# Kernel optimization log

Measured on AMD Instinct MI355X. Metric: run time of the kernel, lower is better.

Reference implementation:

```python
import jax, jax.numpy as jnp
import numpy as np

L, N, IN, H, K, OUT = 512, 256, 256, 512, 2, 256


def setup_inputs() -> dict:
    key = jax.random.key(0)
    ks = jax.random.split(key, 14)
    s = 1.0 / np.sqrt(H)
    u = lambda k, shape: jax.random.uniform(k, shape, jnp.float32, -s, s)
    return {
        'x': jax.random.normal(ks[0], (L, N, IN), jnp.float32),
        'memory': jax.random.normal(ks[1], (N, K * H), jnp.float32) * 0.1,
        'done': jax.random.bernoulli(ks[2], 0.01, (L, N, 1)),
        'Wih0': u(ks[3], (3 * H, IN)),
        'Whh0': u(ks[4], (3 * H, H)),
        'bih0': u(ks[5], (3 * H,)),
        'bhh0': u(ks[6], (3 * H,)),
        'Wih1': u(ks[7], (3 * H, H)),
        'Whh1': u(ks[8], (3 * H, H)),
        'bih1': u(ks[9], (3 * H,)),
        'bhh1': u(ks[10], (3 * H,)),
        'Wp': u(ks[11], (OUT, H)),
        'bp': u(ks[12], (OUT,)),
    }


def _gru_layer(xs, h0, done_f, Wih, Whh, bih, bhh):
    # xs: [L, N, C_in], h0: [N, H], done_f: [L, N, 1] float
    def step(h, inp):
        x_t, d_t = inp
        gi = x_t @ Wih.T + bih            # [N, 3H]
        gh = h @ Whh.T + bhh              # [N, 3H]
        i_r, i_z, i_n = jnp.split(gi, 3, axis=-1)
        h_r, h_z, h_n = jnp.split(gh, 3, axis=-1)
        r = jax.nn.sigmoid(i_r + h_r)
        z = jax.nn.sigmoid(i_z + h_z)
        n = jnp.tanh(i_n + r * h_n)
        h_new = (1.0 - z) * n + z * h     # torch GRU update
        # reset state AFTER an episode terminates at step t (affects t+1)
        h_carry = h_new * (1.0 - d_t)
        return h_carry, h_new
    hT, ys = jax.lax.scan(step, h0, (xs, done_f))
    return ys, hT


def reference(x, memory, done, Wih0, Whh0, bih0, bhh0, Wih1, Whh1, bih1, bhh1, Wp, bp):
    done_f = done.astype(x.dtype)                       # [L, N, 1]
    # memory: 'n (k c) -> k n c'
    h0 = jnp.transpose(memory.reshape(memory.shape[0], K, H), (1, 0, 2))
    y0, h0f = _gru_layer(x, h0[0], done_f, Wih0, Whh0, bih0, bhh0)
    y1, h1f = _gru_layer(y0, h0[1], done_f, Wih1, Whh1, bih1, bhh1)
    # hn: 'k n c -> n (k c)'
    hn = jnp.transpose(jnp.stack([h0f, h1f], 0), (1, 0, 2)).reshape(memory.shape[0], K * H)
    out = y1 @ Wp.T + bp                                # output projection
    return out, hn
```

## Files before the change

kernel.cpp:

```cpp
#include <hip/hip_runtime.h>

static constexpr int LSEQ = 512;
static constexpr int NB   = 256;
static constexpr int CIN  = 256;
static constexpr int HD   = 512;
static constexpr int G3   = 1536;
static constexpr int NOUT = 256;

typedef __attribute__((ext_vector_type(8))) short bf16x8;
typedef __attribute__((ext_vector_type(4))) float f32x4;
typedef __attribute__((ext_vector_type(8))) unsigned short u16x8;
typedef __attribute__((ext_vector_type(4))) unsigned u32x4;

#define DEVI __device__ __forceinline__

DEVI float b2f(unsigned short h) { return __uint_as_float(((unsigned)h) << 16); }
DEVI unsigned short f2b(float x) {
    unsigned u = __float_as_uint(x);
    return (unsigned short)((u + 0x7FFFu + ((u >> 16) & 1u)) >> 16);
}

DEVI unsigned cload(const unsigned* p) {
    return __hip_atomic_load(p, __ATOMIC_RELAXED, __HIP_MEMORY_SCOPE_AGENT);
}
DEVI void cstore(unsigned* p, unsigned v) {
    __hip_atomic_store(p, v, __ATOMIC_RELAXED, __HIP_MEMORY_SCOPE_AGENT);
}

DEVI float fast_tanh(float x) {
    x = fminf(10.f, fmaxf(-10.f, x));
    float e = __expf(-2.f * x);
    return (1.f - e) / (1.f + e);
}

DEVI void cload4x4(const unsigned* p0, const unsigned* p1,
                   const unsigned* p2, const unsigned* p3,
                   u32x4& r0, u32x4& r1, u32x4& r2, u32x4& r3) {
    asm volatile(
        "global_load_dwordx4 %0, %4, off sc0 sc1\n\t"
        "global_load_dwordx4 %1, %5, off sc0 sc1\n\t"
        "global_load_dwordx4 %2, %6, off sc0 sc1\n\t"
        "global_load_dwordx4 %3, %7, off sc0 sc1\n\t"
        "s_waitcnt vmcnt(0)"
        : "=&v"(r0), "=&v"(r1), "=&v"(r2), "=&v"(r3)
        : "v"(p0), "v"(p1), "v"(p2), "v"(p3)
        : "memory");
    __builtin_amdgcn_sched_barrier(0);
}

__global__ void detect_fdt(const unsigned short* __restrict__ x, int nHalf,
                           unsigned* __restrict__ fdt) {
    __shared__ unsigned big;
    if (threadIdx.x == 0) big = 0;
    __syncthreads();
    for (int i = threadIdx.x; i < nHalf; i += 256) {
        unsigned e = (x[i] >> 7) & 0xFFu;
        if (e >= 0xC0u) atomicOr(&big, 1u);
    }
    __syncthreads();
    if (threadIdx.x == 0) *fdt = big ? 1u : 0u;
}

__global__ void cast_bf16(const void* __restrict__ src, long srcOff,
                          unsigned short* __restrict__ dst, long n,
                          const unsigned* __restrict__ fdt) {
    long i = (long)blockIdx.x * 256 + threadIdx.x;
    long stride = (long)gridDim.x * 256;
    if (*fdt) {
        const float* s = (const float*)src + srcOff;
        for (; i < n; i += stride) dst[i] = f2b(s[i]);
    } else {
        const unsigned short* s = (const unsigned short*)src + srcOff;
        for (; i < n; i += stride) dst[i] = s[i];
    }
}

__global__ void detect_done(const unsigned char* __restrict__ d, int elems,
                            unsigned* __restrict__ flag) {
    __shared__ unsigned bad[4];
    int tid = threadIdx.x;
    if (tid < 4) bad[tid] = 0;
    __syncthreads();
    int nInt = elems >> 2;
    const unsigned* di = (const unsigned*)d;
    for (int i = tid; i < nInt; i += 256) {
        unsigned v = di[i];
        if (v > 1u) atomicOr(&bad[0], 1u);
        if (v != 0u && v != 0x3F800000u) atomicOr(&bad[1], 1u);
    }
    int nHalf = elems >> 1;
    const unsigned short* dh = (const unsigned short*)d;
    for (int i = tid; i < nHalf; i += 256) {
        unsigned short h = dh[i];
        if (h != 0 && h != 0x3F80) atomicOr(&bad[2], 1u);
    }
    __syncthreads();
    if (tid == 0) {
        unsigned f;
        if (!bad[0]) f = 0u;
        else if (!bad[1]) f = 3u;
        else if (!bad[2]) f = 2u;
        else f = 1u;
        *flag = f;
    }
}

__global__ void expand_done(const void* __restrict__ d, const unsigned* __restrict__ flag,
                            float* __restrict__ keep, int elems) {
    int i = blockIdx.x * 256 + threadIdx.x;
    if (i >= elems) return;
    unsigned f = *flag;
    float v;
    if (f == 0u)      v = (float)((const int*)d)[i];
    else if (f == 1u) v = (float)((const unsigned char*)d)[i];
    else if (f == 2u) v = b2f(((const unsigned short*)d)[i]);
    else              v = ((const float*)d)[i];
    keep[i] = 1.f - v;
}

__global__ __launch_bounds__(256) void gemm_nt(
    const unsigned short* __restrict__ A, const unsigned short* __restrict__ B,
    const unsigned short* __restrict__ bias, unsigned short* __restrict__ C,
    float* __restrict__ Cf, const unsigned* __restrict__ fdt,
    int M, int N, int K) {
    __shared__ unsigned short sm[16384];
    const int tid = threadIdx.x;
    const int l = tid & 63, w = tid >> 6;
    const int lr = l & 15, lq = l >> 4;
    const int wr = w >> 1, wc = w & 1;
    const long rowBase = (long)blockIdx.y * 128;
    const long colBase = (long)blockIdx.x * 128;

    int qrow[4], qc8[4];
#pragma unroll
    for (int i = 0; i < 4; i++) {
        int q = (i * 4 + w) * 64 + l;
        qrow[i] = q >> 3;
        qc8[i] = (q & 7) * 8;
    }

    f32x4 acc[4][4] = {};

    for (int k0 = 0; k0 < K; k0 += 64) {
#pragma unroll
        for (int i = 0; i < 4; i++) {
            const unsigned short* sA = A + (rowBase + qrow[i]) * K + k0 + qc8[i];
            const unsigned short* sB = B + (colBase + qrow[i]) * K + k0 + qc8[i];
            __builtin_amdgcn_global_load_lds(
                (const __attribute__((address_space(1))) void*)sA,
                (__attribute__((address_space(3))) void*)(sm + (i * 4 + w) * 512), 16, 0, 0);
            __builtin_amdgcn_global_load_lds(
                (const __attribute__((address_space(1))) void*)sB,
                (__attribute__((address_space(3))) void*)(sm + 8192 + (i * 4 + w) * 512), 16, 0, 0);
        }
        __syncthreads();
#pragma unroll
        for (int ks = 0; ks < 2; ks++) {
            bf16x8 af[4], bfr[4];
#pragma unroll
            for (int mi = 0; mi < 4; mi++)
                af[mi] = *(const bf16x8*)&sm[(wr * 64 + mi * 16 + lr) * 64 + ks * 32 + lq * 8];
#pragma unroll
            for (int ni = 0; ni < 4; ni++)
                bfr[ni] = *(const bf16x8*)&sm[8192 + (wc * 64 + ni * 16 + lr) * 64 + ks * 32 + lq * 8];
#pragma unroll
            for (int mi = 0; mi < 4; mi++)
#pragma unroll
                for (int ni = 0; ni < 4; ni++)
                    acc[mi][ni] = __builtin_amdgcn_mfma_f32_16x16x32_bf16(
                        af[mi], bfr[ni], acc[mi][ni], 0, 0, 0);
        }
        __syncthreads();
    }

    float bv[4];
#pragma unroll
    for (int ni = 0; ni < 4; ni++)
        bv[ni] = bias ? b2f(bias[colBase + wc * 64 + ni * 16 + lr]) : 0.f;

    const bool f32out = (fdt != nullptr) && (*fdt != 0u);
    if (f32out) {
#pragma unroll
        for (int mi = 0; mi < 4; mi++)
#pragma unroll
            for (int ni = 0; ni < 4; ni++)
#pragma unroll
                for (int rg = 0; rg < 4; rg++) {
                    int m = wr * 64 + mi * 16 + lq * 4 + rg;
                    int n = wc * 64 + ni * 16 + lr;
                    Cf[(rowBase + m) * (long)N + colBase + n] = acc[mi][ni][rg] + bv[ni];
                }
        return;
    }

#pragma unroll
    for (int mi = 0; mi < 4; mi++)
#pragma unroll
        for (int ni = 0; ni < 4; ni++)
#pragma unroll
            for (int rg = 0; rg < 4; rg++) {
                int m = wr * 64 + mi * 16 + lq * 4 + rg;
                int n = wc * 64 + ni * 16 + lr;
                sm[m * 128 + n] = f2b(acc[mi][ni][rg] + bv[ni]);
            }
    __syncthreads();
#pragma unroll
    for (int i = 0; i < 8; i++) {
        int idx = i * 2048 + tid * 8;
        int r = idx >> 7, c = idx & 127;
        *(u16x8*)(C + (rowBase + r) * N + colBase + c) = *(const u16x8*)&sm[idx];
    }
}

DEVI void gru_body(
    const unsigned short* __restrict__ gi,
    const unsigned short* __restrict__ Whh,
    const unsigned short* __restrict__ bhh,
    const float* __restrict__ keep,
    const unsigned short* __restrict__ mem,
    unsigned short* __restrict__ hdb,
    unsigned short* __restrict__ Y,
    unsigned short* __restrict__ hnB, float* __restrict__ hnF,
    bool f32out, int t0, int Tc, int layerOff,
    unsigned* __restrict__ ctr, int lb) {
    const int tid = threadIdx.x;
    const int l = tid & 63, w = tid >> 6, lr = l & 15, lq = l >> 4;
    const int bi = lb & 15, bj = lb >> 4;

    __shared__ float red[4][16][100];

    bf16x8 wreg[6][4];
#pragma unroll
    for (int fr = 0; fr < 6; fr++) {
        int g = fr >> 1, cf = fr & 1;
        long row = (long)g * HD + bj * 32 + cf * 16 + lr;
#pragma unroll
        for (int ks = 0; ks < 4; ks++) {
            int k = w * 128 + ks * 32 + lq * 8;
            wreg[fr][ks] = *(const bf16x8*)(Whh + row * HD + k);
        }
    }

    const int m = tid >> 4, c0 = (tid & 15) * 2;
    const int n_g = bi * 16 + m;
    const int ch = bj * 32 + c0;
    float bh[3][2];
#pragma unroll
    for (int g = 0; g < 3; g++) {
        unsigned v = *(const unsigned*)(bhh + g * HD + ch);
        bh[g][0] = b2f((unsigned short)(v & 0xffffu));
        bh[g][1] = b2f((unsigned short)(v >> 16));
    }

    if (t0 == 0) {
        unsigned v = *(const unsigned*)(mem + (long)n_g * 1024 + layerOff + ch);
        cstore((unsigned*)(hdb + (long)n_g * HD + ch), v);
        unsigned* islot = ctr + ((long)Tc * 16 + bi) * 32;
        __syncthreads();
        if (tid == 0) {
            __hip_atomic_fetch_add(islot, 1u, __ATOMIC_RELAXED, __HIP_MEMORY_SCOPE_AGENT);
            while (__hip_atomic_load(islot, __ATOMIC_RELAXED, __HIP_MEMORY_SCOPE_AGENT) < 16u)
                __builtin_amdgcn_s_sleep(1);
        }
        __syncthreads();
    }

    float hpv[2];
    {
        unsigned hp0 = cload((const unsigned*)(hdb + (long)(t0 & 1) * NB * HD + (long)n_g * HD + ch));
        hpv[0] = b2f((unsigned short)(hp0 & 0xffffu));
        hpv[1] = b2f((unsigned short)(hp0 >> 16));
    }

    unsigned gv[3];
    float kp;
    {
        const unsigned short* gp = gi + (long)n_g * G3;
#pragma unroll
        for (int g = 0; g < 3; g++) gv[g] = *(const unsigned*)(gp + g * HD + ch);
        kp = keep[(long)t0 * NB + n_g];
    }

    for (int t = t0; t < t0 + Tc; ++t) {
        const unsigned short* hc = hdb + (long)(t & 1) * NB * HD;
        unsigned short* hx = hdb + (long)((t + 1) & 1) * NB * HD;

        const unsigned* hrow = (const unsigned*)(hc + (long)(bi * 16 + lr) * HD);
        union { u32x4 u; bf16x8 v; } t0u, t1u, t2u, t3u;
        cload4x4(hrow + w * 64 + 0 * 16 + lq * 4, hrow + w * 64 + 1 * 16 + lq * 4,
                 hrow + w * 64 + 2 * 16 + lq * 4, hrow + w * 64 + 3 * 16 + lq * 4,
                 t0u.u, t1u.u, t2u.u, t3u.u);
        bf16x8 af[4] = { t0u.v, t1u.v, t2u.v, t3u.v };

        f32x4 acc[6] = {};
#pragma unroll
        for (int ks = 0; ks < 4; ks++)
#pragma unroll
            for (int fr = 0; fr < 6; fr++)
                acc[fr] = __builtin_amdgcn_mfma_f32_16x16x32_bf16(af[ks], wreg[fr][ks], acc[fr], 0, 0, 0);

#pragma unroll
        for (int fr = 0; fr < 6; fr++)
#pragma unroll
            for (int rg = 0; rg < 4; rg++)
                red[w][lq * 4 + rg][fr * 16 + lr] = acc[fr][rg];
        __syncthreads();

        float s[3][2];
#pragma unroll
        for (int g = 0; g < 3; g++) { s[g][0] = 0.f; s[g][1] = 0.f; }
#pragma unroll
        for (int ww = 0; ww < 4; ww++)
#pragma unroll
            for (int g = 0; g < 3; g++) {
                const float* p = &red[ww][m][g * 32 + c0];
                s[g][0] += p[0];
                s[g][1] += p[1];
            }

        unsigned short yo[2], ho[2];
        float hcf[2];
#pragma unroll
        for (int j = 0; j < 2; j++) {
            float ir  = b2f((unsigned short)((gv[0] >> (16 * j)) & 0xffffu));
            float iz  = b2f((unsigned short)((gv[1] >> (16 * j)) & 0xffffu));
            float in_ = b2f((unsigned short)((gv[2] >> (16 * j)) & 0xffffu));
            float r = 1.f / (1.f + __expf(-(ir + s[0][j] + bh[0][j])));
            float z = 1.f / (1.f + __expf(-(iz + s[1][j] + bh[1][j])));
            float nn = fast_tanh(in_ + r * (s[2][j] + bh[2][j]));
            float hnew = (1.f - z) * nn + z * hpv[j];
            hcf[j] = hnew * kp;
            yo[j] = f2b(hnew);
            ho[j] = f2b(hcf[j]);
            hpv[j] = b2f(ho[j]);
        }
        unsigned ypack = (unsigned)yo[0] | ((unsigned)yo[1] << 16);
        unsigned hpack = (unsigned)ho[0] | ((unsigned)ho[1] << 16);

        cstore((unsigned*)(hx + (long)n_g * HD + ch), hpack);

        const bool last = (t + 1 >= t0 + Tc);
        unsigned* slot = ctr + ((long)(t - t0) * 16 + bi) * 32;
        if (!last) {
            __syncthreads();
            if (tid == 0)
                __hip_atomic_fetch_add(slot, 1u, __ATOMIC_RELAXED, __HIP_MEMORY_SCOPE_AGENT);
        }

        *(unsigned*)(Y + ((long)(t - t0) * NB + n_g) * HD + ch) = ypack;
        if (t == LSEQ - 1) {
            if (f32out) {
                hnF[(long)n_g * 1024 + layerOff + ch]     = hcf[0];
                hnF[(long)n_g * 1024 + layerOff + ch + 1] = hcf[1];
            } else {
                *(unsigned*)(hnB + (long)n_g * 1024 + layerOff + ch) = hpack;
            }
        }
        if (!last) {
            const unsigned short* gp = gi + ((long)(t + 1 - t0) * NB + n_g) * G3;
#pragma unroll
            for (int g = 0; g < 3; g++) gv[g] = *(const unsigned*)(gp + g * HD + ch);
            kp = keep[(long)(t + 1) * NB + n_g];
            if (tid == 0) {
                while (__hip_atomic_load(slot, __ATOMIC_RELAXED, __HIP_MEMORY_SCOPE_AGENT) < 16u)
                    __builtin_amdgcn_s_sleep(1);
            }
            __syncthreads();
        }
    }
}

__global__ __launch_bounds__(256, 2) void gru_dual(
    const unsigned short* giA, const unsigned short* WhhA, const unsigned short* bhhA,
    unsigned short* hdbA, unsigned short* YA, int t0A, unsigned* ctrA, int enA,
    const unsigned short* giB, const unsigned short* WhhB, const unsigned short* bhhB,
    unsigned short* hdbB, unsigned short* YB, int t0B, unsigned* ctrB, int enB,
    const float* keep, const unsigned short* mem,
    unsigned short* hnB, float* hnF, const unsigned* fdt, int Tc) {
    const bool f32out = (*fdt != 0u);
    const int half = blockIdx.x >> 8;
    const int lb = blockIdx.x & 255;
    if (half == 0) {
        if (enA) gru_body(giA, WhhA, bhhA, keep, mem, hdbA, YA, hnB, hnF,
                          f32out, t0A, Tc, 0, ctrA, lb);
    } else {
        if (enB) gru_body(giB, WhhB, bhhB, keep, mem, hdbB, YB, hnB, hnF,
                          f32out, t0B, Tc, HD, ctrB, lb);
    }
}

extern "C" void kernel_launch(void* const* d_in, const int* in_sizes, int n_in,
                              void* d_out, int out_size, void* d_ws, size_t ws_size,
                              hipStream_t stream) {
    const void* x    = d_in[0];
    const void* mem  = d_in[1];
    const void* done = d_in[2];
    const void* fsrc[11] = { mem, d_in[3], d_in[4], d_in[5], d_in[6],
                             d_in[7], d_in[8], d_in[9], d_in[10], d_in[11], d_in[12] };
    const long  fn[11]   = { (long)NB * 1024, (long)G3 * CIN, (long)G3 * HD, G3, G3,
                             (long)G3 * HD, (long)G3 * HD, G3, G3, (long)NOUT * HD, NOUT };

    unsigned short* outB = (unsigned short*)d_out;
    float*          outF = (float*)d_out;
    unsigned short* hnB  = outB + (size_t)LSEQ * NB * NOUT;
    float*          hnF  = outF + (size_t)LSEQ * NB * NOUT;

    char* ws = (char*)d_ws;
    const size_t oFlag = 0;
    const size_t oKeep = 256;
    const size_t oCtr  = oKeep + (size_t)LSEQ * NB * 4;
    const size_t oWC   = oCtr + (size_t)8 * 1024 * 1024;
    size_t wcTot = 0;
    size_t wcOff[11];
    for (int i = 0; i < 11; i++) { wcOff[i] = wcTot; wcTot += (size_t)fn[i] * 2; wcTot = (wcTot + 255) & ~(size_t)255; }
    const size_t oHdb0 = oWC + wcTot;
    const size_t oHdb1 = oHdb0 + (size_t)2 * NB * HD * 2;
    const size_t oDyn  = oHdb1 + (size_t)2 * NB * HD * 2;

    int Tc = 4;
    const int cand[6] = {128, 64, 32, 16, 8, 4};
    for (int i = 0; i < 6; i++) {
        size_t need = oDyn + (size_t)cand[i] * NB * (CIN + 2 * G3 + 2 * HD) * 2;
        if (need <= ws_size) { Tc = cand[i]; break; }
    }
    const size_t oXC  = oDyn;
    const size_t oGI0 = oXC + (size_t)Tc * NB * CIN * 2;
    const size_t oGI1 = oGI0 + (size_t)Tc * NB * G3 * 2;
    const size_t oY0c = oGI1 + (size_t)Tc * NB * G3 * 2;
    const size_t oY1c = oY0c + (size_t)Tc * NB * HD * 2;

    unsigned*       FDT  = (unsigned*)(ws + oFlag);
    unsigned*       DFLG = (unsigned*)(ws + oFlag + 64);
    float*          KEEP = (float*)(ws + oKeep);
    unsigned*       CTR  = (unsigned*)(ws + oCtr);
    unsigned short* WC   = (unsigned short*)(ws + oWC);
    unsigned short* HDB0 = (unsigned short*)(ws + oHdb0);
    unsigned short* HDB1 = (unsigned short*)(ws + oHdb1);
    unsigned short* XC   = (unsigned short*)(ws + oXC);
    unsigned short* GI0  = (unsigned short*)(ws + oGI0);
    unsigned short* GI1  = (unsigned short*)(ws + oGI1);
    unsigned short* Y0c  = (unsigned short*)(ws + oY0c);
    unsigned short* Y1c  = (unsigned short*)(ws + oY1c);

    unsigned short* MEMc = WC + wcOff[0] / 2;
    unsigned short* WIH0 = WC + wcOff[1] / 2;
    unsigned short* WHH0 = WC + wcOff[2] / 2;
    unsigned short* BIH0 = WC + wcOff[3] / 2;
    unsigned short* BHH0 = WC + wcOff[4] / 2;
    unsigned short* WIH1 = WC + wcOff[5] / 2;
    unsigned short* WHH1 = WC + wcOff[6] / 2;
    unsigned short* BIH1 = WC + wcOff[7] / 2;
    unsigned short* BHH1 = WC + wcOff[8] / 2;
    unsigned short* WPc  = WC + wcOff[9] / 2;
    unsigned short* BPc  = WC + wcOff[10] / 2;

    hipMemsetAsync(ws + oCtr, 0, (size_t)8 * 1024 * 1024, stream);
    detect_fdt<<<1, 256, 0, stream>>>((const unsigned short*)x, 4096, FDT);
    detect_done<<<1, 256, 0, stream>>>((const unsigned char*)done, in_sizes[2], DFLG);
    expand_done<<<(LSEQ * NB + 255) / 256, 256, 0, stream>>>(done, DFLG, KEEP, LSEQ * NB);

    for (int i = 0; i < 11; i++) {
        int blocks = (int)((fn[i] + 1023) / 1024);
        if (blocks > 2048) blocks = 2048;
        cast_bf16<<<blocks, 256, 0, stream>>>(fsrc[i], 0, WC + wcOff[i] / 2, fn[i], FDT);
    }

    const int NC = LSEQ / Tc;
    const size_t SZ = (size_t)(Tc + 2) * 16 * 32;
    const long giN = (long)Tc * NB * CIN;

    cast_bf16<<<2048, 256, 0, stream>>>(x, 0, XC, giN, FDT);
    gemm_nt<<<dim3(G3 / 128, Tc * NB / 128), 256, 0, stream>>>(
        XC, WIH0, BIH0, GI0, nullptr, nullptr, Tc * NB, G3, CIN);

    for (int it = 0; it <= NC; ++it) {
        const int cA = it, cB = it - 1;
        const int enA = (cA < NC) ? 1 : 0;
        const int enB = (cB >= 0) ? 1 : 0;

        gru_dual<<<512, 256, 0, stream>>>(
            GI0, WHH0, BHH0, HDB0, Y0c, cA * Tc, CTR + (size_t)(2 * it) * SZ, enA,
            GI1, WHH1, BHH1, HDB1, Y1c, cB * Tc, CTR + (size_t)(2 * it + 1) * SZ, enB,
            KEEP, MEMc, hnB, hnF, FDT, Tc);

        if (enA)
            gemm_nt<<<dim3(G3 / 128, Tc * NB / 128), 256, 0, stream>>>(
                Y0c, WIH1, BIH1, GI1, nullptr, nullptr, Tc * NB, G3, HD);
        if (enB)
            gemm_nt<<<dim3(NOUT / 128, Tc * NB / 128), 256, 0, stream>>>(
                Y1c, WPc, BPc, outB + (size_t)cB * Tc * NB * NOUT,
                outF + (size_t)cB * Tc * NB * NOUT, FDT, Tc * NB, NOUT, HD);
        if (cA + 1 < NC) {
            cast_bf16<<<2048, 256, 0, stream>>>(x, (long)(cA + 1) * Tc * NB * CIN, XC, giN, FDT);
            gemm_nt<<<dim3(G3 / 128, Tc * NB / 128), 256, 0, stream>>>(
                XC, WIH0, BIH0, GI0, nullptr, nullptr, Tc * NB, G3, CIN);
        }
    }
}
```

Baseline: 2.448 ms.

## Fuse input-projection GEMMs into the recurrent GRU kernel with register-resident Wih

Result: slower. 2.553 ms (+4.3%).

```diff
diff --git a/kernel.cpp b/kernel.cpp
--- a/kernel.cpp
+++ b/kernel.cpp
@@ -27,6 +27,7 @@
     __hip_atomic_store(p, v, __ATOMIC_RELAXED, __HIP_MEMORY_SCOPE_AGENT);
 }
 
+DEVI float sigm(float v) { return 1.f / (1.f + __expf(-v)); }
 DEVI float fast_tanh(float x) {
     x = fminf(10.f, fmaxf(-10.f, x));
     float e = __expf(-2.f * x);
@@ -212,24 +213,24 @@
     }
 }
 
+template <int KV>
 DEVI void gru_body(
-    const unsigned short* __restrict__ gi,
-    const unsigned short* __restrict__ Whh,
-    const unsigned short* __restrict__ bhh,
-    const float* __restrict__ keep,
-    const unsigned short* __restrict__ mem,
-    unsigned short* __restrict__ hdb,
-    unsigned short* __restrict__ Y,
+    const void* __restrict__ vin,
+    int vF32, int vT0off,
+    const unsigned short* __restrict__ wih,
+    const unsigned short* __restrict__ whh,
+    const unsigned short* __restrict__ bih, const unsigned short* __restrict__ bhh,
+    const float* __restrict__ keep, const unsigned short* __restrict__ mem,
+    unsigned short* __restrict__ hdb, unsigned short* __restrict__ Y,
     unsigned short* __restrict__ hnB, float* __restrict__ hnF,
     bool f32out, int t0, int Tc, int layerOff,
-    unsigned* __restrict__ ctr, int lb) {
+    unsigned* __restrict__ ctr, int lb, float (*red)[16][132]) {
+    constexpr int KVR = KV / 128;
     const int tid = threadIdx.x;
     const int l = tid & 63, w = tid >> 6, lr = l & 15, lq = l >> 4;
     const int bi = lb & 15, bj = lb >> 4;
 
-    __shared__ float red[4][16][100];
-
-    bf16x8 wreg[6][4];
+    bf16x8 wreg[6][4], wi[6][KVR];
 #pragma unroll
     for (int fr = 0; fr < 6; fr++) {
         int g = fr >> 1, cf = fr & 1;
@@ -237,19 +238,28 @@
 #pragma unroll
         for (int ks = 0; ks < 4; ks++) {
             int k = w * 128 + ks * 32 + lq * 8;
-            wreg[fr][ks] = *(const bf16x8*)(Whh + row * HD + k);
+            wreg[fr][ks] = *(const bf16x8*)(whh + row * HD + k);
+        }
+#pragma unroll
+        for (int ks = 0; ks < KVR; ks++) {
+            int k2 = w * (KV / 4) + ks * 32 + lq * 8;
+            wi[fr][ks] = *(const bf16x8*)(wih + row * KV + k2);
         }
     }
 
     const int m = tid >> 4, c0 = (tid & 15) * 2;
     const int n_g = bi * 16 + m;
     const int ch = bj * 32 + c0;
-    float bh[3][2];
-#pragma unroll
-    for (int g = 0; g < 3; g++) {
-        unsigned v = *(const unsigned*)(bhh + g * HD + ch);
-        bh[g][0] = b2f((unsigned short)(v & 0xffffu));
-        bh[g][1] = b2f((unsigned short)(v >> 16));
+    float brz[2][2], bnx[2], bnh[2];
+#pragma unroll
+    for (int g = 0; g < 2; g++)
+#pragma unroll
+        for (int j = 0; j < 2; j++)
+            brz[g][j] = b2f(bih[g * HD + ch + j]) + b2f(bhh[g * HD + ch + j]);
+#pragma unroll
+    for (int j = 0; j < 2; j++) {
+        bnx[j] = b2f(bih[2 * HD + ch + j]);
+        bnh[j] = b2f(bhh[2 * HD + ch + j]);
     }
 
     if (t0 == 0) {
@@ -272,14 +282,32 @@
         hpv[1] = b2f((unsigned short)(hp0 >> 16));
     }
 
-    unsigned gv[3];
+    auto loadV = [&](int t, bf16x8* vf) {
+        long rowoff = ((long)(t - vT0off) * NB + bi * 16 + lr);
+        int kb = w * (KV / 4) + lq * 8;
+        if (!vF32) {
+            const unsigned short* vp = (const unsigned short*)vin + rowoff * KV + kb;
+#pragma unroll
+            for (int i = 0; i < KVR; i++) vf[i] = *(const bf16x8*)(vp + i * 32);
+        } else {
+            const float* vp = (const float*)vin + rowoff * KV + kb;
+#pragma unroll
+            for (int i = 0; i < KVR; i++) {
+                f32x4 a = *(const f32x4*)(vp + i * 32);
+                f32x4 b = *(const f32x4*)(vp + i * 32 + 4);
+#pragma unroll
+                for (int e = 0; e < 4; e++) {
+                    ((unsigned short*)&vf[i])[e]     = f2b(a[e]);
+                    ((unsigned short*)&vf[i])[4 + e] = f2b(b[e]);
+                }
+            }
+        }
+    };
+
+    bf16x8 vf[KVR];
     float kp;
-    {
-        const unsigned short* gp = gi + (long)n_g * G3;
-#pragma unroll
-        for (int g = 0; g < 3; g++) gv[g] = *(const unsigned*)(gp + g * HD + ch);
-        kp = keep[(long)t0 * NB + n_g];
-    }
+    loadV(t0, vf);
+    kp = keep[(long)t0 * NB + n_g];
 
     for (int t = t0; t < t0 + Tc; ++t) {
         const unsigned short* hc = hdb + (long)(t & 1) * NB * HD;
@@ -292,42 +320,48 @@
                  t0u.u, t1u.u, t2u.u, t3u.u);
         bf16x8 af[4] = { t0u.v, t1u.v, t2u.v, t3u.v };
 
-        f32x4 acc[6] = {};
+        f32x4 acc[8] = {};
 #pragma unroll
         for (int ks = 0; ks < 4; ks++)
 #pragma unroll
-            for (int fr = 0; fr < 6; fr++)
-                acc[fr] = __builtin_amdgcn_mfma_f32_16x16x32_bf16(af[ks], wreg[fr][ks], acc[fr], 0, 0, 0);
-
-#pragma unroll
-        for (int fr = 0; fr < 6; fr++)
+            for (int fr = 0; fr < 6; fr++) {
+                int g = fr >> 1, cf = fr & 1;
+                int dst = (g < 2) ? fr : (4 + cf);
+                acc[dst] = __builtin_amdgcn_mfma_f32_16x16x32_bf16(af[ks], wreg[fr][ks], acc[dst], 0, 0, 0);
+            }
+#pragma unroll
+        for (int ks = 0; ks < KVR; ks++)
+#pragma unroll
+            for (int fr = 0; fr < 6; fr++) {
+                int g = fr >> 1, cf = fr & 1;
+                int dst = (g < 2) ? fr : (6 + cf);
+                acc[dst] = __builtin_amdgcn_mfma_f32_16x16x32_bf16(vf[ks], wi[fr][ks], acc[dst], 0, 0, 0);
+            }
+
+#pragma unroll
+        for (int f = 0; f < 8; f++)
 #pragma unroll
             for (int rg = 0; rg < 4; rg++)
-                red[w][lq * 4 + rg][fr * 16 + lr] = acc[fr][rg];
+                red[w][lq * 4 + rg][f * 16 + lr] = acc[f][rg];
         __syncthreads();
 
-        float s[3][2];
-#pragma unroll
-        for (int g = 0; g < 3; g++) { s[g][0] = 0.f; s[g][1] = 0.f; }
-#pragma unroll
-        for (int ww = 0; ww < 4; ww++)
-#pragma unroll
-            for (int g = 0; g < 3; g++) {
-                const float* p = &red[ww][m][g * 32 + c0];
-                s[g][0] += p[0];
-                s[g][1] += p[1];
-            }
+        float sr[2] = {0, 0}, sz[2] = {0, 0}, snh[2] = {0, 0}, snx[2] = {0, 0};
+#pragma unroll
+        for (int ww = 0; ww < 4; ww++) {
+            const float* p = &red[ww][m][0];
+            sr[0] += p[c0];       sr[1] += p[c0 + 1];
+            sz[0] += p[32 + c0];  sz[1] += p[33 + c0];
+            snh[0] += p[64 + c0]; snh[1] += p[65 + c0];
+            snx[0] += p[96 + c0]; snx[1] += p[97 + c0];
+        }
 
         unsigned short yo[2], ho[2];
         float hcf[2];
 #pragma unroll
         for (int j = 0; j < 2; j++) {
-            float ir  = b2f((unsigned short)((gv[0] >> (16 * j)) & 0xffffu));
-            float iz  = b2f((unsigned short)((gv[1] >> (16 * j)) & 0xffffu));
-            float in_ = b2f((unsigned short)((gv[2] >> (16 * j)) & 0xffffu));
-            float r = 1.f / (1.f + __expf(-(ir + s[0][j] + bh[0][j])));
-            float z = 1.f / (1.f + __expf(-(iz + s[1][j] + bh[1][j])));
-            float nn = fast_tanh(in_ + r * (s[2][j] + bh[2][j]));
+            float r = sigm(sr[j] + brz[0][j]);
+            float z = sigm(sz[j] + brz[1][j]);
+            float nn = fast_tanh((snx[j] + bnx[j]) + r * (snh[j] + bnh[j]));
             float hnew = (1.f - z) * nn + z * hpv[j];
             hcf[j] = hnew * kp;
             yo[j] = f2b(hnew);
@@ -357,9 +391,7 @@
             }
         }
         if (!last) {
-            const unsigned short* gp = gi + ((long)(t + 1 - t0) * NB + n_g) * G3;
-#pragma unroll
-            for (int g = 0; g < 3; g++) gv[g] = *(const unsigned*)(gp + g * HD + ch);
+            loadV(t + 1, vf);
             kp = keep[(long)(t + 1) * NB + n_g];
             if (tid == 0) {
                 while (__hip_atomic_load(slot, __ATOMIC_RELAXED, __HIP_MEMORY_SCOPE_AGENT) < 16u)
@@ -371,21 +403,28 @@
 }
 
 __global__ __launch_bounds__(256, 2) void gru_dual(
-    const unsigned short* giA, const unsigned short* WhhA, const unsigned short* bhhA,
+    const void* xin,
+    const unsigned short* WIH0, const unsigned short* WHH0,
+    const unsigned short* BIH0, const unsigned short* BHH0,
     unsigned short* hdbA, unsigned short* YA, int t0A, unsigned* ctrA, int enA,
-    const unsigned short* giB, const unsigned short* WhhB, const unsigned short* bhhB,
+    const unsigned short* y0prev,
+    const unsigned short* WIH1, const unsigned short* WHH1,
+    const unsigned short* BIH1, const unsigned short* BHH1,
     unsigned short* hdbB, unsigned short* YB, int t0B, unsigned* ctrB, int enB,
     const float* keep, const unsigned short* mem,
     unsigned short* hnB, float* hnF, const unsigned* fdt, int Tc) {
+    __shared__ float red[4][16][132];
     const bool f32out = (*fdt != 0u);
     const int half = blockIdx.x >> 8;
     const int lb = blockIdx.x & 255;
     if (half == 0) {
-        if (enA) gru_body(giA, WhhA, bhhA, keep, mem, hdbA, YA, hnB, hnF,
-                          f32out, t0A, Tc, 0, ctrA, lb);
+        if (enA) gru_body<CIN>(xin, f32out ? 1 : 0, 0, WIH0, WHH0, BIH0, BHH0,
+                               keep, mem, hdbA, YA, hnB, hnF, f32out,
+                               t0A, Tc, 0, ctrA, lb, red);
     } else {
-        if (enB) gru_body(giB, WhhB, bhhB, keep, mem, hdbB, YB, hnB, hnF,
-                          f32out, t0B, Tc, HD, ctrB, lb);
+        if (enB) gru_body<HD>(y0prev, 0, t0B, WIH1, WHH1, BIH1, BHH1,
+                              keep, mem, hdbB, YB, hnB, hnF, f32out,
+                              t0B, Tc, HD, ctrB, lb, red);
     }
 }
 
@@ -420,14 +459,12 @@
     int Tc = 4;
     const int cand[6] = {128, 64, 32, 16, 8, 4};
     for (int i = 0; i < 6; i++) {
-        size_t need = oDyn + (size_t)cand[i] * NB * (CIN + 2 * G3 + 2 * HD) * 2;
+        size_t need = oDyn + (size_t)3 * cand[i] * NB * HD * 2;
         if (need <= ws_size) { Tc = cand[i]; break; }
     }
-    const size_t oXC  = oDyn;
-    const size_t oGI0 = oXC + (size_t)Tc * NB * CIN * 2;
-    const size_t oGI1 = oGI0 + (size_t)Tc * NB * G3 * 2;
-    const size_t oY0c = oGI1 + (size_t)Tc * NB * G3 * 2;
-    const size_t oY1c = oY0c + (size_t)Tc * NB * HD * 2;
+    const size_t oY0A = oDyn;
+    const size_t oY0B = oY0A + (size_t)Tc * NB * HD * 2;
+    const size_t oY1  = oY0B + (size_t)Tc * NB * HD * 2;
 
     unsigned*       FDT  = (unsigned*)(ws + oFlag);
     unsigned*       DFLG = (unsigned*)(ws + oFlag + 64);
@@ -436,11 +473,9 @@
     unsigned short* WC   = (unsigned short*)(ws + oWC);
     unsigned short* HDB0 = (unsigned short*)(ws + oHdb0);
     unsigned short* HDB1 = (unsigned short*)(ws + oHdb1);
-    unsigned short* XC   = (unsigned short*)(ws + oXC);
-    unsigned short* GI0  = (unsigned short*)(ws + oGI0);
-    unsigned short* GI1  = (unsigned short*)(ws + oGI1);
-    unsigned short* Y0c  = (unsigned short*)(ws + oY0c);
-    unsigned short* Y1c  = (unsigned short*)(ws + oY1c);
+    unsigned short* Y0A  = (unsigned short*)(ws + oY0A);
+    unsigned short* Y0B  = (unsigned short*)(ws + oY0B);
+    unsigned short* Y1c  = (unsigned short*)(ws + oY1);
 
     unsigned short* MEMc = WC + wcOff[0] / 2;
     unsigned short* WIH0 = WC + wcOff[1] / 2;
@@ -467,33 +502,24 @@
 
     const int NC = LSEQ / Tc;
     const size_t SZ = (size_t)(Tc + 2) * 16 * 32;
-    const long giN = (long)Tc * NB * CIN;
-
-    cast_bf16<<<2048, 256, 0, stream>>>(x, 0, XC, giN, FDT);
-    gemm_nt<<<dim3(G3 / 128, Tc * NB / 128), 256, 0, stream>>>(
-        XC, WIH0, BIH0, GI0, nullptr, nullptr, Tc * NB, G3, CIN);
 
     for (int it = 0; it <= NC; ++it) {
         const int cA = it, cB = it - 1;
         const int enA = (cA < NC) ? 1 : 0;
         const int enB = (cB >= 0) ? 1 : 0;
+        unsigned short* YA = (cA & 1) ? Y0B : Y0A;
+        const unsigned short* VB = (cB & 1) ? Y0B : Y0A;
 
         gru_dual<<<512, 256, 0, stream>>>(
-            GI0, WHH0, BHH0, HDB0, Y0c, cA * Tc, CTR + (size_t)(2 * it) * SZ, enA,
-            GI1, WHH1, BHH1, HDB1, Y1c, cB * Tc, CTR + (size_t)(2 * it + 1) * SZ, enB,
+            x, WIH0, WHH0, BIH0, BHH0, HDB0, YA, cA * Tc,
+            CTR + (size_t)(2 * it) * SZ, enA,
+            VB, WIH1, WHH1, BIH1, BHH1, HDB1, Y1c, cB * Tc,
+            CTR + (size_t)(2 * it + 1) * SZ, enB,
             KEEP, MEMc, hnB, hnF, FDT, Tc);
 
-        if (enA)
-            gemm_nt<<<dim3(G3 / 128, Tc * NB / 128), 256, 0, stream>>>(
-                Y0c, WIH1, BIH1, GI1, nullptr, nullptr, Tc * NB, G3, HD);
         if (enB)
             gemm_nt<<<dim3(NOUT / 128, Tc * NB / 128), 256, 0, stream>>>(
                 Y1c, WPc, BPc, outB + (size_t)cB * Tc * NB * NOUT,
                 outF + (size_t)cB * Tc * NB * NOUT, FDT, Tc * NB, NOUT, HD);
-        if (cA + 1 < NC) {
-            cast_bf16<<<2048, 256, 0, stream>>>(x, (long)(cA + 1) * Tc * NB * CIN, XC, giN, FDT);
-            gemm_nt<<<dim3(G3 / 128, Tc * NB / 128), 256, 0, stream>>>(
-                XC, WIH0, BIH0, GI0, nullptr, nullptr, Tc * NB, G3, CIN);
-        }
-    }
-}
+    }
+}
```
